# Performance work log

Measured on AMD Instinct MI355X. Metric: run time of the kernel, lower is better.

The kernel has to match this reference:

```python
import math
import jax, jax.numpy as jnp
import numpy as np

K = 128  # num_kernels
H = 32   # num_heads
MAX_NODE_TYPE = 100
B = 4    # num graphs
N_PER_G = 512


def setup_inputs() -> dict:
    key = jax.random.key(0)
    ks = jax.random.split(key, 10)
    coord = jax.random.normal(ks[0], (B * N_PER_G, 3), dtype=jnp.float32)
    node_type = jax.random.randint(ks[1], (B * N_PER_G,), 0, MAX_NODE_TYPE + 1)
    gaussian_means = jax.random.uniform(ks[2], (1, K), minval=0.0, maxval=3.0, dtype=jnp.float32)
    gaussian_stds = jax.random.uniform(ks[3], (1, K), minval=0.0, maxval=3.0, dtype=jnp.float32)
    mul_w = jnp.zeros((MAX_NODE_TYPE + 1, 2), dtype=jnp.float32)   # init.constant_(mul, 0)
    bias_w = jnp.ones((MAX_NODE_TYPE + 1, 2), dtype=jnp.float32)   # init.constant_(bias, 1)
    W1 = jax.random.normal(ks[4], (K, K), dtype=jnp.float32) / math.sqrt(K)
    b1 = jax.random.normal(ks[5], (K,), dtype=jnp.float32) * 0.01
    W2 = jax.random.normal(ks[6], (H, K), dtype=jnp.float32) / math.sqrt(K)
    b2 = jax.random.normal(ks[7], (H,), dtype=jnp.float32) * 0.01
    return {
        "coord": coord, "node_type": node_type,
        "gaussian_means": gaussian_means, "gaussian_stds": gaussian_stds,
        "mul_w": mul_w, "bias_w": bias_w,
        "W1": W1, "b1": b1, "W2": W2, "b2": b2,
        "num_graphs": B, "num_nodes": N_PER_G,
    }


def _encode_graph(xg, ntg, mu, var, mul_w, bias_w, W1, b1, W2, b2):
    # xg: [n,3], ntg: [n]
    diff = xg[:, None, :] - xg[None, :, :]
    d2 = jnp.sum(diff * diff, axis=-1)                       # [n,n]
    dist = jnp.where(d2 > 0, jnp.sqrt(jnp.where(d2 > 0, d2, 1.0)), 0.0)
    me = mul_w[ntg]                                           # [n,2]
    be = bias_w[ntg]
    mul = me[:, 0][:, None] + me[None, :, 1]                  # [n,n]
    bias = be[:, 0][:, None] + be[None, :, 1]
    scaled = (mul * dist + bias)[..., None]                   # [n,n,K]
    gk = jnp.exp(-0.5 * jnp.square((scaled - mu) / var)) / (-math.sqrt(2.0 * math.pi) * var)
    h = jax.nn.gelu(gk @ W1.T + b1, approximate=False)        # exact GELU as in torch default
    return h @ W2.T + b2                                      # [n,n,H]


def reference(coord, node_type, gaussian_means, gaussian_stds, mul_w, bias_w,
              W1, b1, W2, b2, num_graphs, num_nodes):
    x = coord.reshape(num_graphs, num_nodes, 3)
    nt = node_type.reshape(num_graphs, num_nodes)
    mu = gaussian_means.reshape(-1)                           # [K]
    var = jnp.abs(gaussian_stds.reshape(-1)) + 0.01           # [K]
    enc = lambda xg, ntg: _encode_graph(xg, ntg, mu, var, mul_w, bias_w, W1, b1, W2, b2)
    return jax.vmap(enc)(x, nt)                               # [B,n,n,H]
```

## Files before the change

### kernel.cpp

```cpp
#include <hip/hip_runtime.h>

#define NGRAPH 4
#define NNODE  512
#define NTOT   2048
#define KK     128
#define HH     32
#define TAB_T  4096
#define NPAIR  (NGRAPH*NNODE*NNODE)
#define MMB    1024

#define BLK_OFF  16
#define NODE_OFF (BLK_OFF + 2*MMB)
#define W1T_OFF  (NODE_OFF + NTOT*8)
#define W2T_OFF  (W1T_OFF + KK*KK)
#define B1_OFF   (W2T_OFF + KK*HH)
#define B2_OFF   (B1_OFF + KK)
#define MU_OFF   (B2_OFF + HH)
#define VAR_OFF  (MU_OFF + KK)
#define TAB_OFF  39424

__device__ __forceinline__ float bf2f(unsigned short h) {
    return __uint_as_float(((unsigned)h) << 16);
}
__device__ __forceinline__ unsigned short f2bf(float f) {
    unsigned u = __float_as_uint(f);
    u += 0x7FFFu + ((u >> 16) & 1u);
    return (unsigned short)(u >> 16);
}
__device__ __forceinline__ unsigned pk2(float a, float b) {
    return (unsigned)f2bf(a) | ((unsigned)f2bf(b) << 16);
}
__device__ __forceinline__ float ldf(const void* p, int i, bool bf) {
    return bf ? bf2f(((const unsigned short*)p)[i]) : ((const float*)p)[i];
}
__device__ __forceinline__ float gelu_exact(float x) {
    return x * 0.5f * (1.0f + erff(x * 0.7071067811865476f));
}
__device__ __forceinline__ float pair_s(const float* __restrict__ ws, int g, int i, int j) {
    const float4* ri = (const float4*)(ws + NODE_OFF + (size_t)(g*NNODE + i)*8);
    const float4* rj = (const float4*)(ws + NODE_OFF + (size_t)(g*NNODE + j)*8);
    const float4 ai = ri[0], bi = ri[1];
    const float4 aj = rj[0], bj = rj[1];
    const float dx = ai.x - aj.x, dy = ai.y - aj.y, dz = ai.z - aj.z;
    const float d2 = dx*dx + dy*dy + dz*dz;
    const float dist = (d2 > 0.0f) ? sqrtf(d2) : 0.0f;
    return (ai.w + bj.x) * dist + (bi.y + bj.z);
}

__global__ void k_prep(const void* coord, const int* __restrict__ ntype,
                       const void* means, const void* stds,
                       const void* mulw, const void* biasw,
                       const void* W1, const void* b1,
                       const void* W2, const void* b2,
                       float* __restrict__ ws) {
    const bool bf = (((const unsigned*)biasw)[0] == 0x3F803F80u);
    const int t = blockIdx.x * blockDim.x + threadIdx.x;
    if (t < NTOT) {
        const int nt = ntype[t];
        float* rec = ws + NODE_OFF + t * 8;
        rec[0] = ldf(coord, t*3+0, bf);
        rec[1] = ldf(coord, t*3+1, bf);
        rec[2] = ldf(coord, t*3+2, bf);
        rec[3] = ldf(mulw,  nt*2+0, bf);
        rec[4] = ldf(mulw,  nt*2+1, bf);
        rec[5] = ldf(biasw, nt*2+0, bf);
        rec[6] = ldf(biasw, nt*2+1, bf);
        rec[7] = 0.0f;
    } else if (t < NTOT + KK*KK) {
        const int m = t - NTOT;
        const int k = m >> 7, j = m & (KK-1);
        ws[W1T_OFF + m] = ldf(W1, j*KK + k, bf);
    } else if (t < NTOT + KK*KK + KK*HH) {
        const int m = t - NTOT - KK*KK;
        const int j = m >> 5, ch = m & (HH-1);
        ws[W2T_OFF + m] = ldf(W2, ch*KK + j, bf);
    } else if (t < NTOT + KK*KK + KK*HH + KK) {
        const int m = t - NTOT - KK*KK - KK*HH;
        ws[B1_OFF + m] = ldf(b1, m, bf);
    } else if (t < NTOT + KK*KK + KK*HH + KK + HH) {
        const int m = t - NTOT - KK*KK - KK*HH - KK;
        ws[B2_OFF + m] = ldf(b2, m, bf);
    } else if (t < NTOT + KK*KK + KK*HH + KK + HH + KK) {
        const int m = t - NTOT - KK*KK - KK*HH - KK - HH;
        ws[MU_OFF + m] = ldf(means, m, bf);
    } else if (t < NTOT + KK*KK + KK*HH + KK + HH + 2*KK) {
        const int m = t - NTOT - KK*KK - KK*HH - KK - HH - KK;
        ws[VAR_OFF + m] = fabsf(ldf(stds, m, bf)) + 0.01f;
    }
}

__global__ __launch_bounds__(256) void k_minmax(float* __restrict__ ws) {
    __shared__ float smn[4], smx[4];
    float mn = 1e30f, mx = -1e30f;
    for (int p = blockIdx.x * 256 + threadIdx.x; p < NPAIR; p += MMB * 256) {
        const int j = p & (NNODE-1);
        const int i = (p >> 9) & (NNODE-1);
        const int g = p >> 18;
        const float s = pair_s(ws, g, i, j);
        mn = fminf(mn, s); mx = fmaxf(mx, s);
    }
    #pragma unroll
    for (int off = 32; off > 0; off >>= 1) {
        mn = fminf(mn, __shfl_xor(mn, off, 64));
        mx = fmaxf(mx, __shfl_xor(mx, off, 64));
    }
    const int wv = threadIdx.x >> 6;
    if ((threadIdx.x & 63) == 0) { smn[wv] = mn; smx[wv] = mx; }
    __syncthreads();
    if (threadIdx.x == 0) {
        mn = fminf(fminf(smn[0], smn[1]), fminf(smn[2], smn[3]));
        mx = fmaxf(fmaxf(smx[0], smx[1]), fmaxf(smx[2], smx[3]));
        ws[BLK_OFF + 2*blockIdx.x]     = mn;
        ws[BLK_OFF + 2*blockIdx.x + 1] = mx;
    }
}

__global__ __launch_bounds__(128) void k_table(float* __restrict__ ws) {
    __shared__ float g_s[KK][4];
    __shared__ float h_s[4][KK];
    __shared__ float wmn[2], wmx[2];
    const int tid = threadIdx.x;

    float mn = 1e30f, mx = -1e30f;
    for (int b = tid; b < MMB; b += 128) {
        mn = fminf(mn, ws[BLK_OFF + 2*b]);
        mx = fmaxf(mx, ws[BLK_OFF + 2*b + 1]);
    }
    #pragma unroll
    for (int off = 32; off > 0; off >>= 1) {
        mn = fminf(mn, __shfl_xor(mn, off, 64));
        mx = fmaxf(mx, __shfl_xor(mx, off, 64));
    }
    if ((tid & 63) == 0) { wmn[tid >> 6] = mn; wmx[tid >> 6] = mx; }
    __syncthreads();
    const float lo = fminf(wmn[0], wmn[1]);
    const float hi = fmaxf(wmx[0], wmx[1]);
    if (blockIdx.x == 0 && tid == 0) { ws[0] = lo; ws[1] = hi; }

    float width = hi - lo;
    if (!(width > 1e-6f)) width = 1e-6f;
    const float step = width * (1.0f / (float)(TAB_T - 1));
    const int e0 = blockIdx.x * 4;

    {
        const float mu  = ws[MU_OFF + tid];
        const float var = ws[VAR_OFF + tid];
        const float inv = 1.0f / var;
        const float amp = -0.3989422804014327f * inv;
        #pragma unroll
        for (int e = 0; e < 4; ++e) {
            const float s = lo + (float)(e0 + e) * step;
            const float z = (s - mu) * inv;
            g_s[tid][e] = amp * expf(-0.5f * z * z);
        }
    }
    __syncthreads();
    float a0 = ws[B1_OFF + tid], a1 = a0, a2 = a0, a3 = a0;
    for (int k = 0; k < KK; ++k) {
        const float w = ws[W1T_OFF + k*KK + tid];
        const float4 gv = *(const float4*)g_s[k];
        a0 += w * gv.x; a1 += w * gv.y; a2 += w * gv.z; a3 += w * gv.w;
    }
    h_s[0][tid] = gelu_exact(a0);
    h_s[1][tid] = gelu_exact(a1);
    h_s[2][tid] = gelu_exact(a2);
    h_s[3][tid] = gelu_exact(a3);
    __syncthreads();
    const int e = tid >> 5, ch = tid & (HH-1);
    float acc = ws[B2_OFF + ch];
    for (int j = 0; j < KK; ++j)
        acc += ws[W2T_OFF + j*HH + ch] * h_s[e][j];
    ws[TAB_OFF + (size_t)(e0 + e)*HH + ch] = acc;
}

__global__ __launch_bounds__(256) void k_apply(const float* __restrict__ ws,
                                               const void* __restrict__ biasw,
                                               void* __restrict__ out) {
    const bool bf = (((const unsigned*)biasw)[0] == 0x3F803F80u);
    const int gid = blockIdx.x * blockDim.x + threadIdx.x;
    const int q = gid & 3;
    const int p = gid >> 2;
    const int j = p & (NNODE-1);
    const int i = (p >> 9) & (NNODE-1);
    const int g = p >> 18;
    const float s = pair_s(ws, g, i, j);

    const float lo = ws[0], hi = ws[1];
    float width = hi - lo;
    if (!(width > 1e-6f)) width = 1e-6f;
    float u = (s - lo) * ((float)(TAB_T - 1) / width);
    u = fminf(fmaxf(u, 0.0f), (float)(TAB_T - 1));
    int i0 = (int)u;
    if (i0 > TAB_T - 2) i0 = TAB_T - 2;
    const float f = u - (float)i0;

    const float4* t0 = (const float4*)(ws + TAB_OFF + (size_t)i0 * HH);
    const float4 a0 = t0[2*q],     c0 = t0[2*q + 8];
    const float4 a1 = t0[2*q + 1], c1 = t0[2*q + 9];
    const float r0 = a0.x + f*(c0.x - a0.x), r1 = a0.y + f*(c0.y - a0.y);
    const float r2 = a0.z + f*(c0.z - a0.z), r3 = a0.w + f*(c0.w - a0.w);
    const float r4 = a1.x + f*(c1.x - a1.x), r5 = a1.y + f*(c1.y - a1.y);
    const float r6 = a1.z + f*(c1.z - a1.z), r7 = a1.w + f*(c1.w - a1.w);
    if (bf) {
        uint4 w;
        w.x = pk2(r0, r1); w.y = pk2(r2, r3);
        w.z = pk2(r4, r5); w.w = pk2(r6, r7);
        ((uint4*)((unsigned short*)out + (size_t)p * HH))[q] = w;
    } else {
        float4* op = (float4*)((float*)out + (size_t)p * HH) + 2*q;
        op[0] = make_float4(r0, r1, r2, r3);
        op[1] = make_float4(r4, r5, r6, r7);
    }
}

extern "C" void kernel_launch(void* const* d_in, const int* in_sizes, int n_in,
                              void* d_out, int out_size, void* d_ws, size_t ws_size,
                              hipStream_t stream) {
    const void* coord = d_in[0];
    const int*  ntype = (const int*)d_in[1];
    const void* means = d_in[2];
    const void* stds  = d_in[3];
    const void* mulw  = d_in[4];
    const void* biasw = d_in[5];
    const void* W1    = d_in[6];
    const void* b1    = d_in[7];
    const void* W2    = d_in[8];
    const void* b2    = d_in[9];
    float* ws = (float*)d_ws;

    k_prep<<<90, 256, 0, stream>>>(coord, ntype, means, stds, mulw, biasw, W1, b1, W2, b2, ws);
    k_minmax<<<MMB, 256, 0, stream>>>(ws);
    k_table<<<TAB_T/4, 128, 0, stream>>>(ws);
    k_apply<<<(NPAIR*4)/256, 256, 0, stream>>>(ws, biasw, d_out);
}
```

Baseline: 182.9 us.

## Replace exact pairwise min/max pass with per-node bounding-box range bound

Drops the k_minmax kernel, which evaluated every pair's scaled distance to find the lookup-table range. Per-wave min/max of coordinates and type weights are now computed in k_prep, and k_table derives a conservative bound from a per-graph bounding-box diagonal and the weight extremes. This removes one launch and a full pass over a million pairs. The looser range may coarsen table resolution and change accuracy.

```diff
diff --git a/kernel.cpp b/kernel.cpp
--- a/kernel.cpp
+++ b/kernel.cpp
@@ -7,10 +7,9 @@
 #define HH     32
 #define TAB_T  4096
 #define NPAIR  (NGRAPH*NNODE*NNODE)
-#define MMB    1024
-
-#define BLK_OFF  16
-#define NODE_OFF (BLK_OFF + 2*MMB)
+
+#define STAT_OFF 16
+#define NODE_OFF 2064
 #define W1T_OFF  (NODE_OFF + NTOT*8)
 #define W2T_OFF  (W1T_OFF + KK*KK)
 #define B1_OFF   (W2T_OFF + KK*HH)
@@ -57,15 +56,32 @@
     const int t = blockIdx.x * blockDim.x + threadIdx.x;
     if (t < NTOT) {
         const int nt = ntype[t];
+        const float x  = ldf(coord, t*3+0, bf);
+        const float y  = ldf(coord, t*3+1, bf);
+        const float z  = ldf(coord, t*3+2, bf);
+        const float m0 = ldf(mulw,  nt*2+0, bf);
+        const float m1 = ldf(mulw,  nt*2+1, bf);
+        const float b0 = ldf(biasw, nt*2+0, bf);
+        const float b1v= ldf(biasw, nt*2+1, bf);
         float* rec = ws + NODE_OFF + t * 8;
-        rec[0] = ldf(coord, t*3+0, bf);
-        rec[1] = ldf(coord, t*3+1, bf);
-        rec[2] = ldf(coord, t*3+2, bf);
-        rec[3] = ldf(mulw,  nt*2+0, bf);
-        rec[4] = ldf(mulw,  nt*2+1, bf);
-        rec[5] = ldf(biasw, nt*2+0, bf);
-        rec[6] = ldf(biasw, nt*2+1, bf);
-        rec[7] = 0.0f;
+        rec[0] = x;  rec[1] = y;  rec[2] = z;  rec[3] = m0;
+        rec[4] = m1; rec[5] = b0; rec[6] = b1v; rec[7] = 0.0f;
+
+        float mn[7] = {m0, m1, b0, b1v, x, y, z};
+        float mx[7] = {m0, m1, b0, b1v, x, y, z};
+        #pragma unroll
+        for (int off = 32; off > 0; off >>= 1) {
+            #pragma unroll
+            for (int q = 0; q < 7; ++q) {
+                mn[q] = fminf(mn[q], __shfl_xor(mn[q], off, 64));
+                mx[q] = fmaxf(mx[q], __shfl_xor(mx[q], off, 64));
+            }
+        }
+        if ((threadIdx.x & 63) == 0) {
+            float* sp = ws + STAT_OFF + (size_t)((blockIdx.x << 2) + (threadIdx.x >> 6)) * 16;
+            #pragma unroll
+            for (int q = 0; q < 7; ++q) { sp[q] = mn[q]; sp[7 + q] = mx[q]; }
+        }
     } else if (t < NTOT + KK*KK) {
         const int m = t - NTOT;
         const int k = m >> 7, j = m & (KK-1);
@@ -89,53 +105,49 @@
     }
 }
 
-__global__ __launch_bounds__(256) void k_minmax(float* __restrict__ ws) {
-    __shared__ float smn[4], smx[4];
-    float mn = 1e30f, mx = -1e30f;
-    for (int p = blockIdx.x * 256 + threadIdx.x; p < NPAIR; p += MMB * 256) {
-        const int j = p & (NNODE-1);
-        const int i = (p >> 9) & (NNODE-1);
-        const int g = p >> 18;
-        const float s = pair_s(ws, g, i, j);
-        mn = fminf(mn, s); mx = fmaxf(mx, s);
-    }
-    #pragma unroll
-    for (int off = 32; off > 0; off >>= 1) {
-        mn = fminf(mn, __shfl_xor(mn, off, 64));
-        mx = fmaxf(mx, __shfl_xor(mx, off, 64));
-    }
-    const int wv = threadIdx.x >> 6;
-    if ((threadIdx.x & 63) == 0) { smn[wv] = mn; smx[wv] = mx; }
-    __syncthreads();
-    if (threadIdx.x == 0) {
-        mn = fminf(fminf(smn[0], smn[1]), fminf(smn[2], smn[3]));
-        mx = fmaxf(fmaxf(smx[0], smx[1]), fmaxf(smx[2], smx[3]));
-        ws[BLK_OFF + 2*blockIdx.x]     = mn;
-        ws[BLK_OFF + 2*blockIdx.x + 1] = mx;
-    }
-}
-
 __global__ __launch_bounds__(128) void k_table(float* __restrict__ ws) {
     __shared__ float g_s[KK][4];
     __shared__ float h_s[4][KK];
-    __shared__ float wmn[2], wmx[2];
+    __shared__ float sh_lo, sh_hi;
     const int tid = threadIdx.x;
 
-    float mn = 1e30f, mx = -1e30f;
-    for (int b = tid; b < MMB; b += 128) {
-        mn = fminf(mn, ws[BLK_OFF + 2*b]);
-        mx = fmaxf(mx, ws[BLK_OFF + 2*b + 1]);
-    }
-    #pragma unroll
-    for (int off = 32; off > 0; off >>= 1) {
-        mn = fminf(mn, __shfl_xor(mn, off, 64));
-        mx = fmaxf(mx, __shfl_xor(mx, off, 64));
-    }
-    if ((tid & 63) == 0) { wmn[tid >> 6] = mn; wmx[tid >> 6] = mx; }
+    if (tid < 32) {
+        const float* sp = ws + STAT_OFF + tid * 16;
+        float m0n = sp[0], m1n = sp[1], b0n = sp[2], b1n = sp[3];
+        float xn  = sp[4], yn  = sp[5], zn  = sp[6];
+        float m0x = sp[7], m1x = sp[8], b0x = sp[9], b1x = sp[10];
+        float xx  = sp[11], yx = sp[12], zx = sp[13];
+        #pragma unroll
+        for (int off = 1; off < 8; off <<= 1) {
+            xn = fminf(xn, __shfl_xor(xn, off, 64)); xx = fmaxf(xx, __shfl_xor(xx, off, 64));
+            yn = fminf(yn, __shfl_xor(yn, off, 64)); yx = fmaxf(yx, __shfl_xor(yx, off, 64));
+            zn = fminf(zn, __shfl_xor(zn, off, 64)); zx = fmaxf(zx, __shfl_xor(zx, off, 64));
+        }
+        const float dx = xx - xn, dy = yx - yn, dz = zx - zn;
+        float dmax2 = dx*dx + dy*dy + dz*dz;
+        #pragma unroll
+        for (int off = 8; off < 32; off <<= 1)
+            dmax2 = fmaxf(dmax2, __shfl_xor(dmax2, off, 64));
+        #pragma unroll
+        for (int off = 1; off < 32; off <<= 1) {
+            m0n = fminf(m0n, __shfl_xor(m0n, off, 64)); m0x = fmaxf(m0x, __shfl_xor(m0x, off, 64));
+            m1n = fminf(m1n, __shfl_xor(m1n, off, 64)); m1x = fmaxf(m1x, __shfl_xor(m1x, off, 64));
+            b0n = fminf(b0n, __shfl_xor(b0n, off, 64)); b0x = fmaxf(b0x, __shfl_xor(b0x, off, 64));
+            b1n = fminf(b1n, __shfl_xor(b1n, off, 64)); b1x = fmaxf(b1x, __shfl_xor(b1x, off, 64));
+        }
+        if (tid == 0) {
+            const float dmax = sqrtf(dmax2);
+            const float mlo = m0n + m1n, mhi = m0x + m1x;
+            const float pl = fminf(0.0f, fminf(mlo * dmax, mhi * dmax));
+            const float ph = fmaxf(0.0f, fmaxf(mlo * dmax, mhi * dmax));
+            const float lo = pl + b0n + b1n;
+            const float hi = ph + b0x + b1x;
+            sh_lo = lo; sh_hi = hi;
+            if (blockIdx.x == 0) { ws[0] = lo; ws[1] = hi; }
+        }
+    }
     __syncthreads();
-    const float lo = fminf(wmn[0], wmn[1]);
-    const float hi = fmaxf(wmx[0], wmx[1]);
-    if (blockIdx.x == 0 && tid == 0) { ws[0] = lo; ws[1] = hi; }
+    const float lo = sh_lo, hi = sh_hi;
 
     float width = hi - lo;
     if (!(width > 1e-6f)) width = 1e-6f;
@@ -229,7 +241,6 @@
     float* ws = (float*)d_ws;
 
     k_prep<<<90, 256, 0, stream>>>(coord, ntype, means, stds, mulw, biasw, W1, b1, W2, b2, ws);
-    k_minmax<<<MMB, 256, 0, stream>>>(ws);
     k_table<<<TAB_T/4, 128, 0, stream>>>(ws);
     k_apply<<<(NPAIR*4)/256, 256, 0, stream>>>(ws, biasw, d_out);
 }
```

Measured after the change: 176.1 us. 3.7% less time.
